# Performance work log

Hardware: AMD Instinct MI355X
Metric: run time of the kernel (lower is better)

The kernel has to match this reference:

```python
import jax, jax.numpy as jnp
import numpy as np

B, T, D, H, L, DFF, MAXLEN = 4, 2048, 512, 8, 6, 2048, 2048
DK = D // H
SCALE = float(1.0 / np.sqrt(DK * 2))  # 1/sqrt(d_k*2)


def layer_norm(x, g, b, eps=1e-5):
    m = jnp.mean(x, axis=-1, keepdims=True)
    v = jnp.var(x, axis=-1, keepdims=True)
    return (x - m) / jnp.sqrt(v + eps) * g + b


def setup_inputs() -> dict:
    key = jax.random.key(0)
    it = iter(jax.random.split(key, 48))
    def n(shape, std=0.02):
        return jax.random.normal(next(it), shape, dtype=jnp.float32) * std
    inp = {}
    inp['x'] = jax.random.normal(next(it), (B, T), dtype=jnp.float32)
    inp['ip_w'] = n((1, D)); inp['ip_b'] = jnp.zeros((D,))
    inp['ip_ln_g'] = jnp.ones((D,)); inp['ip_ln_b'] = jnp.zeros((D,))
    inp['pos_embed'] = n((MAXLEN, D), 0.01)
    inp['pad_token'] = n((D,), 0.01)
    inp['Wq'] = n((L, D, D)); inp['bq'] = jnp.zeros((L, D))
    inp['Wk'] = n((L, D, D)); inp['bk'] = jnp.zeros((L, D))
    inp['Wv'] = n((L, D, D)); inp['bv'] = jnp.zeros((L, D))
    inp['Wo'] = n((L, D, D)); inp['bo'] = jnp.zeros((L, D))
    inp['ln1_g'] = jnp.ones((L, D)); inp['ln1_b'] = jnp.zeros((L, D))
    inp['ln2_g'] = jnp.ones((L, D)); inp['ln2_b'] = jnp.zeros((L, D))
    inp['W1'] = n((L, D, DFF)); inp['b1'] = jnp.zeros((L, DFF))
    inp['W2'] = n((L, DFF, D)); inp['b2'] = jnp.zeros((L, D))
    inp['gate1'] = jnp.full((L,), 0.1); inp['gate2'] = jnp.full((L,), 0.1)
    inp['fn_g'] = jnp.ones((D,)); inp['fn_b'] = jnp.zeros((D,))
    for p in ['bh', 'ah', 'ch']:
        inp[p + '_ln_g'] = jnp.ones((D,)); inp[p + '_ln_b'] = jnp.zeros((D,))
    inp['bh_w'] = n((D, 2), 0.01); inp['bh_b'] = jnp.zeros((2,))
    inp['ah_w'] = n((D, 1), 0.01); inp['ah_b'] = jnp.zeros((1,))
    inp['ch_w'] = n((D, 1), 0.01); inp['ch_b'] = jnp.zeros((1,))
    return inp


def _forward(x, ip_w, ip_b, ip_ln_g, ip_ln_b, pos_embed, pad_token,
             Wq, bq, Wk, bk, Wv, bv, Wo, bo,
             ln1_g, ln1_b, ln2_g, ln2_b, W1, b1, W2, b2, gate1, gate2,
             fn_g, fn_b, bh_ln_g, bh_ln_b, bh_w, bh_b,
             ah_ln_g, ah_ln_b, ah_w, ah_b, ch_ln_g, ch_ln_b, ch_w, ch_b):
    Bx, Tx = x.shape
    xc = jnp.clip(x, -10.0, 10.0)
    pad_mask = xc == -1.0  # [B,T]
    h = layer_norm(xc[..., None] @ ip_w + ip_b, ip_ln_g, ip_ln_b)  # [B,T,D]
    h = h + 0.1 * pos_embed[None, :Tx, :]
    h = jnp.where(pad_mask[..., None], pad_token, h)
    cmask = jnp.triu(jnp.full((Tx, Tx), -10000.0, dtype=h.dtype), k=1)  # additive causal mask
    for i in range(L):
        xn = layer_norm(h, ln1_g[i], ln1_b[i])
        def heads(w, b, xn=xn):
            return (xn @ w + b).reshape(Bx, Tx, H, DK).transpose(0, 2, 1, 3)
        q = heads(Wq[i], bq[i]); k = heads(Wk[i], bk[i]); v = heads(Wv[i], bv[i])
        q = q / jnp.maximum(jnp.linalg.norm(q, axis=-1, keepdims=True), 1e-8)
        k = k / jnp.maximum(jnp.linalg.norm(k, axis=-1, keepdims=True), 1e-8)
        scores = jnp.clip(jnp.einsum('bhtd,bhsd->bhts', q, k) * SCALE, -5.0, 5.0) + cmask
        a = jax.nn.softmax(scores / 1.5, axis=-1)
        o = jnp.einsum('bhts,bhsd->bhtd', a, v).transpose(0, 2, 1, 3).reshape(Bx, Tx, D)
        h = h + gate1[i] * ((o @ Wo[i] + bo[i]) * 0.5)
        xn2 = layer_norm(h, ln2_g[i], ln2_b[i])
        ffn = jax.nn.gelu(xn2 @ W1[i] + b1[i], approximate=False) @ W2[i] + b2[i]
        h = jnp.clip(h + gate2[i] * ffn, -10.0, 10.0)
    h = layer_norm(h, fn_g, fn_b)
    m = (~pad_mask).astype(h.dtype)[..., None]
    mean = (h * m).sum(axis=1) / jnp.maximum(m.sum(axis=1), 1.0)  # masked mean pool [B,D]
    binary = layer_norm(mean, bh_ln_g, bh_ln_b) @ bh_w + bh_b
    anomaly = layer_norm(mean, ah_ln_g, ah_ln_b) @ ah_w + ah_b
    caustic = jax.nn.sigmoid(layer_norm(mean, ch_ln_g, ch_ln_b) @ ch_w + ch_b)
    return jnp.concatenate([binary, anomaly, caustic], axis=-1)  # [B,4]


def reference(x, ip_w, ip_b, ip_ln_g, ip_ln_b, pos_embed, pad_token,
              Wq, bq, Wk, bk, Wv, bv, Wo, bo,
              ln1_g, ln1_b, ln2_g, ln2_b, W1, b1, W2, b2, gate1, gate2,
              fn_g, fn_b, bh_ln_g, bh_ln_b, bh_w, bh_b,
              ah_ln_g, ah_ln_b, ah_w, ah_b, ch_ln_g, ch_ln_b, ch_w, ch_b):
    return _forward(x, ip_w, ip_b, ip_ln_g, ip_ln_b, pos_embed, pad_token,
                    Wq, bq, Wk, bk, Wv, bv, Wo, bo,
                    ln1_g, ln1_b, ln2_g, ln2_b, W1, b1, W2, b2, gate1, gate2,
                    fn_g, fn_b, bh_ln_g, bh_ln_b, bh_w, bh_b,
                    ah_ln_g, ah_ln_b, ah_w, ah_b, ch_ln_g, ch_ln_b, ch_w, ch_b)
```

## Files before the change

kernel.cpp:

```cpp
#include <hip/hip_runtime.h>
#include <math.h>

constexpr int Bsz = 4, T = 2048, D = 512, H = 8, Lnum = 6, DFF = 2048, DK = 64;
constexpr int QS2 = 1024;
constexpr float SCALE = 0.08838834764831845f;
constexpr float K2 = 0.08838834764831845f / 1.5f;

typedef __attribute__((ext_vector_type(8))) short svec8;
typedef __attribute__((ext_vector_type(4))) float fvec4;

__device__ __forceinline__ fvec4 mfma16(svec8 a, svec8 b, fvec4 c) {
    return __builtin_amdgcn_mfma_f32_16x16x32_bf16(a, b, c, 0, 0, 0);
}
__device__ __forceinline__ unsigned short f2b(float f) {
    unsigned int u = __float_as_uint(f);
    u += 0x7fffu + ((u >> 16) & 1u);
    return (unsigned short)(u >> 16);
}
__device__ __forceinline__ float wave_red_sum(float v) {
    for (int o = 32; o > 0; o >>= 1) v += __shfl_down(v, o, 64);
    return __shfl(v, 0, 64);
}
__device__ __forceinline__ void glds16(const unsigned short* g, unsigned short* l) {
    __builtin_amdgcn_global_load_lds(
        (const __attribute__((address_space(1))) unsigned int*)g,
        (__attribute__((address_space(3))) unsigned int*)l, 16, 0, 0);
}
#define FRAG(buf, row, kq) (*(const svec8*)((buf) + (((row) << 6) | ((((kq) ^ ((row) & 7))) << 3))))

__global__ __launch_bounds__(64)
void embed_kernel(const float* __restrict__ x, const float* __restrict__ ip_w,
                  const float* __restrict__ ip_b, const float* __restrict__ g,
                  const float* __restrict__ bta, const float* __restrict__ pos,
                  const float* __restrict__ pad_tok, float* __restrict__ h)
{
    int row = blockIdx.x;
    int t = row & (T - 1);
    int lane = threadIdx.x;
    float xv = x[row];
    float xc = fminf(fmaxf(xv, -10.f), 10.f);
    bool pad = (xc == -1.0f);
    float pre[8];
    float s = 0.f, s2 = 0.f;
#pragma unroll
    for (int j = 0; j < 8; j++) {
        int d = j * 64 + lane;
        float p = xc * ip_w[d] + ip_b[d];
        pre[j] = p; s += p; s2 += p * p;
    }
    s = wave_red_sum(s); s2 = wave_red_sum(s2);
    float m = s * (1.f / 512.f);
    float var = s2 * (1.f / 512.f) - m * m;
    float rstd = 1.f / sqrtf(var + 1e-5f);
#pragma unroll
    for (int j = 0; j < 8; j++) {
        int d = j * 64 + lane;
        float hv = (pre[j] - m) * rstd * g[d] + bta[d] + 0.1f * pos[(size_t)t * D + d];
        if (pad) hv = pad_tok[d];
        h[(size_t)row * D + d] = hv;
    }
}

__global__ __launch_bounds__(256)
void ln_kernel(const float* __restrict__ in, float* __restrict__ out,
               const float* __restrict__ g, const float* __restrict__ b)
{
    int row = blockIdx.x * 4 + (threadIdx.x >> 6);
    int lane = threadIdx.x & 63;
    const float* r = in + (size_t)row * D;
    float4 v0 = ((const float4*)r)[lane];
    float4 v1 = ((const float4*)r)[lane + 64];
    float s = v0.x + v0.y + v0.z + v0.w + v1.x + v1.y + v1.z + v1.w;
    float s2 = v0.x*v0.x + v0.y*v0.y + v0.z*v0.z + v0.w*v0.w
             + v1.x*v1.x + v1.y*v1.y + v1.z*v1.z + v1.w*v1.w;
    s = wave_red_sum(s); s2 = wave_red_sum(s2);
    float m = s * (1.f / 512.f);
    float var = s2 * (1.f / 512.f) - m * m;
    float rstd = 1.f / sqrtf(var + 1e-5f);
    float4 g0 = ((const float4*)g)[lane], g1 = ((const float4*)g)[lane + 64];
    float4 b0 = ((const float4*)b)[lane], b1 = ((const float4*)b)[lane + 64];
    float4 o0, o1;
    o0.x = (v0.x - m) * rstd * g0.x + b0.x; o0.y = (v0.y - m) * rstd * g0.y + b0.y;
    o0.z = (v0.z - m) * rstd * g0.z + b0.z; o0.w = (v0.w - m) * rstd * g0.w + b0.w;
    o1.x = (v1.x - m) * rstd * g1.x + b1.x; o1.y = (v1.y - m) * rstd * g1.y + b1.y;
    o1.z = (v1.z - m) * rstd * g1.z + b1.z; o1.w = (v1.w - m) * rstd * g1.w + b1.w;
    ((float4*)(out + (size_t)row * D))[lane] = o0;
    ((float4*)(out + (size_t)row * D))[lane + 64] = o1;
}

__global__ __launch_bounds__(256)
void ln_bf16_kernel(const float* __restrict__ in, unsigned short* __restrict__ out,
                    const float* __restrict__ g, const float* __restrict__ b)
{
    int row = blockIdx.x * 4 + (threadIdx.x >> 6);
    int lane = threadIdx.x & 63;
    const float* r = in + (size_t)row * D;
    float4 v0 = ((const float4*)r)[lane];
    float4 v1 = ((const float4*)r)[lane + 64];
    float s = v0.x + v0.y + v0.z + v0.w + v1.x + v1.y + v1.z + v1.w;
    float s2 = v0.x*v0.x + v0.y*v0.y + v0.z*v0.z + v0.w*v0.w
             + v1.x*v1.x + v1.y*v1.y + v1.z*v1.z + v1.w*v1.w;
    s = wave_red_sum(s); s2 = wave_red_sum(s2);
    float m = s * (1.f / 512.f);
    float var = s2 * (1.f / 512.f) - m * m;
    float rstd = 1.f / sqrtf(var + 1e-5f);
    float4 g0 = ((const float4*)g)[lane], g1 = ((const float4*)g)[lane + 64];
    float4 b0 = ((const float4*)b)[lane], b1 = ((const float4*)b)[lane + 64];
    unsigned short o0[4], o1[4];
    o0[0] = f2b((v0.x - m) * rstd * g0.x + b0.x); o0[1] = f2b((v0.y - m) * rstd * g0.y + b0.y);
    o0[2] = f2b((v0.z - m) * rstd * g0.z + b0.z); o0[3] = f2b((v0.w - m) * rstd * g0.w + b0.w);
    o1[0] = f2b((v1.x - m) * rstd * g1.x + b1.x); o1[1] = f2b((v1.y - m) * rstd * g1.y + b1.y);
    o1[2] = f2b((v1.z - m) * rstd * g1.z + b1.z); o1[3] = f2b((v1.w - m) * rstd * g1.w + b1.w);
    *(uint2*)(out + (size_t)row * D + lane * 4) = *(uint2*)o0;
    *(uint2*)(out + (size_t)row * D + 256 + lane * 4) = *(uint2*)o1;
}

__global__ __launch_bounds__(256)
void wconv_kernel(const float* __restrict__ wq, const float* __restrict__ wk,
                  const float* __restrict__ wv, const float* __restrict__ wo,
                  const float* __restrict__ w1, const float* __restrict__ w2,
                  unsigned short* __restrict__ oq, unsigned short* __restrict__ ok,
                  unsigned short* __restrict__ ov, unsigned short* __restrict__ oo,
                  unsigned short* __restrict__ o1, unsigned short* __restrict__ o2)
{
    __shared__ float tile[32][33];
    int bid = blockIdx.x;
    const float* in; unsigned short* out; int K, N, kt, nt;
    if (bid < 1024) {
        int sel = bid >> 8, loc = bid & 255;
        in  = sel == 0 ? wq : sel == 1 ? wk : sel == 2 ? wv : wo;
        out = sel == 0 ? oq : sel == 1 ? ok : sel == 2 ? ov : oo;
        K = 512; N = 512; kt = loc >> 4; nt = loc & 15;
    } else if (bid < 2048) {
        int loc = bid - 1024; in = w1; out = o1; K = 512; N = 2048; kt = loc >> 6; nt = loc & 63;
    } else {
        int loc = bid - 2048; in = w2; out = o2; K = 2048; N = 512; kt = loc >> 4; nt = loc & 15;
    }
    int k0 = kt * 32, n0 = nt * 32;
    int t = threadIdx.x;
    int kr = t >> 3, nc = (t & 7) * 4;
    float4 v = *(const float4*)(in + (size_t)(k0 + kr) * N + n0 + nc);
    tile[kr][nc] = v.x; tile[kr][nc + 1] = v.y; tile[kr][nc + 2] = v.z; tile[kr][nc + 3] = v.w;
    __syncthreads();
    unsigned short o[4];
#pragma unroll
    for (int i = 0; i < 4; i++) o[i] = f2b(tile[nc + i][kr]);
    *(uint2*)(out + (size_t)(n0 + kr) * K + k0 + nc) = *(uint2*)o;
}

template<int EPI, int OBF, int BM>
__global__ __launch_bounds__(256)
void gemm_bf16(const unsigned short* __restrict__ A, const unsigned short* __restrict__ BT,
               const float* __restrict__ bias, const float* __restrict__ bias_b,
               const float* __restrict__ bias_c, const float* __restrict__ res,
               void* __restrict__ Cv, unsigned short* __restrict__ vtout,
               int M, int N, int K, const float* __restrict__ gate_p)
{
    constexpr int WN = (BM == 128) ? 2 : 4;
    constexpr int WSPAN = 128 / WN;
    constexpr int NT = WSPAN / 16;
    constexpr int MT = 4;
    constexpr int ACALLS = BM / 32;
    __shared__ __align__(16) unsigned short As[BM * 64];
    __shared__ __align__(16) unsigned short Bs[128 * 64];
    const int tid = threadIdx.x, w = tid >> 6, lane = tid & 63, quad = lane >> 4, ln = lane & 15;
    const int wm = w / WN, wn = w % WN;
    const int m0 = blockIdx.y * BM, n0 = blockIdx.x * 128;
    const int jg = (lane & 7) ^ ((lane >> 3) & 7);
    const int rb = w * 8 + (lane >> 3);
    const unsigned short* Agl = A + (size_t)(m0 + rb) * K + jg * 8;
    const unsigned short* Bgl = BT + (size_t)(n0 + rb) * K + jg * 8;

    fvec4 acc[MT][NT];
#pragma unroll
    for (int mt = 0; mt < MT; mt++)
#pragma unroll
        for (int nt = 0; nt < NT; nt++)
#pragma unroll
            for (int r = 0; r < 4; r++) acc[mt][nt][r] = 0.f;

    for (int k0 = 0; k0 < K; k0 += 64) {
        __syncthreads();
#pragma unroll
        for (int c = 0; c < ACALLS; c++)
            glds16(Agl + k0 + (size_t)c * 32 * K, As + c * 2048 + w * 512);
#pragma unroll
        for (int c = 0; c < 4; c++)
            glds16(Bgl + k0 + (size_t)c * 32 * K, Bs + c * 2048 + w * 512);
        __syncthreads();
#pragma unroll
        for (int kk = 0; kk < 2; kk++) {
            svec8 af[MT], bfr[NT];
#pragma unroll
            for (int mt = 0; mt < MT; mt++)
                af[mt] = FRAG(As, wm * 64 + mt * 16 + ln, kk * 4 + quad);
#pragma unroll
            for (int nt = 0; nt < NT; nt++)
                bfr[nt] = FRAG(Bs, wn * WSPAN + nt * 16 + ln, kk * 4 + quad);
#pragma unroll
            for (int mt = 0; mt < MT; mt++)
#pragma unroll
                for (int nt = 0; nt < NT; nt++)
                    acc[mt][nt] = mfma16(af[mt], bfr[nt], acc[mt][nt]);
        }
    }

    const float gate = (EPI == 1 || EPI == 3) ? gate_p[0] : 0.f;
    float bb[NT];
#pragma unroll
    for (int nt = 0; nt < NT; nt++) {
        int n = n0 + wn * WSPAN + nt * 16 + ln;
        if (EPI == 0) {
            int nseg = n >> 9;
            const float* bsel = nseg == 0 ? bias : (nseg == 1 ? bias_b : bias_c);
            bb[nt] = bsel[n - nseg * 512];
        } else {
            bb[nt] = bias[n];
        }
    }
    const bool qkn = (EPI == 0) && ((n0 + wn * WSPAN) < 1024);
#pragma unroll
    for (int mt = 0; mt < MT; mt++) {
        float v[NT][4];
#pragma unroll
        for (int nt = 0; nt < NT; nt++)
#pragma unroll
            for (int r = 0; r < 4; r++) v[nt][r] = acc[mt][nt][r] + bb[nt];
        if (qkn) {
#pragma unroll
            for (int r = 0; r < 4; r++) {
                float s = 0.f;
#pragma unroll
                for (int nt = 0; nt < NT; nt++) s += v[nt][r] * v[nt][r];
                s += __shfl_xor(s, 1); s += __shfl_xor(s, 2);
                s += __shfl_xor(s, 4); s += __shfl_xor(s, 8);
                float rs = 1.f / fmaxf(sqrtf(s), 1e-8f);
#pragma unroll
                for (int nt = 0; nt < NT; nt++) v[nt][r] *= rs;
            }
        }
#pragma unroll
        for (int nt = 0; nt < NT; nt++) {
            int n = n0 + wn * WSPAN + nt * 16 + ln;
#pragma unroll
            for (int r = 0; r < 4; r++) {
                int m = m0 + wm * 64 + mt * 16 + quad * 4 + r;
                float val = v[nt][r];
                if (EPI == 0) {
                    if (n < 1024) ((unsigned short*)Cv)[(size_t)m * QS2 + n] = f2b(val);
                    else vtout[((size_t)((m >> 11) * 512 + (n - 1024))) * T + (m & (T - 1))] = f2b(val);
                } else {
                    size_t off = (size_t)m * N + n;
                    if (EPI == 1) val = res[off] + gate * 0.5f * val;
                    else if (EPI == 2) val = 0.5f * val * (1.f + erff(val * 0.70710678118654752f));
                    else if (EPI == 3) val = fminf(fmaxf(res[off] + gate * val, -10.f), 10.f);
                    if (OBF) ((unsigned short*)Cv)[off] = f2b(val);
                    else ((float*)Cv)[off] = val;
                }
            }
        }
    }
}

__device__ __forceinline__ void attn_step(
    const unsigned short* Q, unsigned short* Ps, const unsigned short* Ks, const unsigned short* Vt,
    bool diag, fvec4 (&oacc)[4], float (&lp)[4], int w, int quad, int ln)
{
    svec8 a0 = FRAG(Q, w * 16 + ln, quad);
    svec8 a1 = FRAG(Q, w * 16 + ln, 4 + quad);
    fvec4 s[4];
#pragma unroll
    for (int nt = 0; nt < 4; nt++) {
#pragma unroll
        for (int r = 0; r < 4; r++) s[nt][r] = 0.f;
        s[nt] = mfma16(a0, FRAG(Ks, nt * 16 + ln, quad), s[nt]);
        s[nt] = mfma16(a1, FRAG(Ks, nt * 16 + ln, 4 + quad), s[nt]);
    }
    const int qrow = w * 16 + quad * 4;
#pragma unroll
    for (int nt = 0; nt < 4; nt++) {
        int col = nt * 16 + ln;
#pragma unroll
        for (int r = 0; r < 4; r++) {
            float y = s[nt][r] * K2;
            float p = fmaf(y, fmaf(y, fmaf(y, 0.16666667f, 0.5f), 1.f), 1.f);
            if (diag && col > qrow + r) p = 0.f;
            lp[r] += p;
            int row = qrow + r;
            Ps[(row << 6) | ((((col >> 3) ^ (row & 7))) << 3) | (col & 7)] = f2b(p);
        }
    }
#pragma unroll
    for (int ks = 0; ks < 2; ks++) {
        svec8 pa = FRAG(Ps, w * 16 + ln, ks * 4 + quad);
#pragma unroll
        for (int nt = 0; nt < 4; nt++)
            oacc[nt] = mfma16(pa, FRAG(Vt, nt * 16 + ln, ks * 4 + quad), oacc[nt]);
    }
}

__global__ __launch_bounds__(256)
void attn_pair_kernel(const unsigned short* __restrict__ qkv, const unsigned short* __restrict__ vt,
                      unsigned short* __restrict__ o)
{
    __shared__ __align__(16) unsigned short QA[4096], QB[4096];
    __shared__ __align__(16) unsigned short K0[4096], V0[4096], K1[4096], V1[4096];
    __shared__ __align__(16) unsigned short Ps[4096];
    const int p = blockIdx.x, bh = blockIdx.y, b = bh >> 3, hh = bh & 7;
    const int qtA = p, qtB = 31 - p, nst = 32 - p;
    const int tid = threadIdx.x, w = tid >> 6, lane = tid & 63, quad = lane >> 4, ln = lane & 15;
    const int rl = lane >> 3, sl = lane & 7, jgz = sl ^ rl;
    const int w8 = w * 8;
    const int grow = w8 + rl;
    const unsigned short* qrow_p = qkv + ((size_t)(b * T) + grow) * QS2 + hh * 64 + jgz * 8;
    const unsigned short* krow_p = qrow_p + 512;
    const unsigned short* vrow_p = vt + ((size_t)(bh * 64) + grow) * T + jgz * 8;

    glds16(qrow_p + (size_t)(qtA * 64) * QS2, QA + w8 * 64);
    glds16(qrow_p + (size_t)(qtA * 64 + 32) * QS2, QA + (w8 + 32) * 64);
    glds16(qrow_p + (size_t)(qtB * 64) * QS2, QB + w8 * 64);
    glds16(qrow_p + (size_t)(qtB * 64 + 32) * QS2, QB + (w8 + 32) * 64);

    fvec4 oA[4], oB[4];
    float lA[4] = {0, 0, 0, 0}, lB[4] = {0, 0, 0, 0};
#pragma unroll
    for (int nt = 0; nt < 4; nt++)
#pragma unroll
        for (int r = 0; r < 4; r++) { oA[nt][r] = 0.f; oB[nt][r] = 0.f; }

    const int Nph = (nst + 1) >> 1;
    for (int ph = 0; ph < Nph; ph++) {
        const int s0 = 2 * ph, s1 = 2 * ph + 1;
        __syncthreads();
        glds16(krow_p + (size_t)(s0 * 64) * QS2, K0 + w8 * 64);
        glds16(krow_p + (size_t)(s0 * 64 + 32) * QS2, K0 + (w8 + 32) * 64);
        glds16(vrow_p + s0 * 64, V0 + w8 * 64);
        glds16(vrow_p + (size_t)32 * T + s0 * 64, V0 + (w8 + 32) * 64);
        if (s1 < nst) {
            glds16(krow_p + (size_t)(s1 * 64) * QS2, K1 + w8 * 64);
            glds16(krow_p + (size_t)(s1 * 64 + 32) * QS2, K1 + (w8 + 32) * 64);
            glds16(vrow_p + s1 * 64, V1 + w8 * 64);
            glds16(vrow_p + (size_t)32 * T + s1 * 64, V1 + (w8 + 32) * 64);
        }
        __syncthreads();
        attn_step(QB, Ps, K0, V0, s0 == nst - 1, oB, lB, w, quad, ln);
        if (s0 <= p) attn_step(QA, Ps, K0, V0, s0 == p, oA, lA, w, quad, ln);
        if (s1 < nst) {
            attn_step(QB, Ps, K1, V1, s1 == nst - 1, oB, lB, w, quad, ln);
            if (s1 <= p) attn_step(QA, Ps, K1, V1, s1 == p, oA, lA, w, quad, ln);
        }
    }

#pragma unroll
    for (int r = 0; r < 4; r++) {
        float ta = lA[r], tb = lB[r];
        ta += __shfl_xor(ta, 1); ta += __shfl_xor(ta, 2); ta += __shfl_xor(ta, 4); ta += __shfl_xor(ta, 8);
        tb += __shfl_xor(tb, 1); tb += __shfl_xor(tb, 2); tb += __shfl_xor(tb, 4); tb += __shfl_xor(tb, 8);
        lA[r] = ta; lB[r] = tb;
    }
    unsigned short* ogA = o + (size_t)(b * T + qtA * 64 + w * 16 + quad * 4) * D + hh * 64;
    unsigned short* ogB = o + (size_t)(b * T + qtB * 64 + w * 16 + quad * 4) * D + hh * 64;
#pragma unroll
    for (int r = 0; r < 4; r++) {
        float ia = 1.f / lA[r], ib = 1.f / lB[r];
#pragma unroll
        for (int nt = 0; nt < 4; nt++) {
            ogA[(size_t)r * D + nt * 16 + ln] = f2b(oA[nt][r] * ia);
            ogB[(size_t)r * D + nt * 16 + ln] = f2b(oB[nt][r] * ib);
        }
    }
}

__global__ __launch_bounds__(256)
void pool_kernel(const float* __restrict__ hn, const float* __restrict__ x, float* __restrict__ part)
{
    int b = blockIdx.x, ch = blockIdx.y, tid = threadIdx.x;
    int t0 = ch * 128;
    float s0 = 0.f, s1 = 0.f, cnt = 0.f;
    for (int tt = 0; tt < 128; tt++) {
        int t = t0 + tt;
        float xv = x[b * T + t];
        float m = (xv == -1.0f) ? 0.f : 1.f;
        cnt += m;
        const float* r = hn + ((size_t)(b * T + t)) * D;
        s0 += r[tid] * m;
        s1 += r[tid + 256] * m;
    }
    float* pr = part + (size_t)(b * 16 + ch) * 513;
    pr[tid] = s0; pr[tid + 256] = s1;
    if (tid == 0) pr[512] = cnt;
}

__global__ __launch_bounds__(64)
void head_kernel(const float* __restrict__ part,
                 const float* __restrict__ bh_g, const float* __restrict__ bh_bl,
                 const float* __restrict__ ah_g, const float* __restrict__ ah_bl,
                 const float* __restrict__ ch_g, const float* __restrict__ ch_bl,
                 const float* __restrict__ bh_w, const float* __restrict__ bh_b2,
                 const float* __restrict__ ah_w, const float* __restrict__ ah_b2,
                 const float* __restrict__ ch_w, const float* __restrict__ ch_b2,
                 float* __restrict__ out)
{
    int b = blockIdx.x, lane = threadIdx.x;
    float cnt = 0.f;
    for (int c = 0; c < 16; c++) cnt += part[(size_t)(b * 16 + c) * 513 + 512];
    float denom = fmaxf(cnt, 1.f);
    float md[8];
    float s = 0.f, s2 = 0.f;
#pragma unroll
    for (int j = 0; j < 8; j++) {
        int d = j * 64 + lane;
        float acc = 0.f;
        for (int c = 0; c < 16; c++) acc += part[(size_t)(b * 16 + c) * 513 + d];
        md[j] = acc / denom;
        s += md[j]; s2 += md[j] * md[j];
    }
    s = wave_red_sum(s); s2 = wave_red_sum(s2);
    float mu = s * (1.f / 512.f);
    float var = s2 * (1.f / 512.f) - mu * mu;
    float rstd = 1.f / sqrtf(var + 1e-5f);
    float a0 = 0.f, a1 = 0.f, a2 = 0.f, a3 = 0.f;
#pragma unroll
    for (int j = 0; j < 8; j++) {
        int d = j * 64 + lane;
        float z = (md[j] - mu) * rstd;
        float zb = z * bh_g[d] + bh_bl[d];
        a0 += zb * bh_w[d * 2 + 0];
        a1 += zb * bh_w[d * 2 + 1];
        a2 += (z * ah_g[d] + ah_bl[d]) * ah_w[d];
        a3 += (z * ch_g[d] + ch_bl[d]) * ch_w[d];
    }
    a0 = wave_red_sum(a0); a1 = wave_red_sum(a1);
    a2 = wave_red_sum(a2); a3 = wave_red_sum(a3);
    if (lane == 0) {
        out[b * 4 + 0] = a0 + bh_b2[0];
        out[b * 4 + 1] = a1 + bh_b2[1];
        out[b * 4 + 2] = a2 + ah_b2[0];
        float t3 = a3 + ch_b2[0];
        out[b * 4 + 3] = 1.f / (1.f + expf(-t3));
    }
}

extern "C" void kernel_launch(void* const* d_in, const int* in_sizes, int n_in,
                              void* d_out, int out_size, void* d_ws, size_t ws_size,
                              hipStream_t stream)
{
    const float* x      = (const float*)d_in[0];
    const float* ip_w   = (const float*)d_in[1];
    const float* ip_b   = (const float*)d_in[2];
    const float* ip_ln_g= (const float*)d_in[3];
    const float* ip_ln_b= (const float*)d_in[4];
    const float* pos    = (const float*)d_in[5];
    const float* pad_tok= (const float*)d_in[6];
    const float* Wq = (const float*)d_in[7];  const float* bq = (const float*)d_in[8];
    const float* Wk = (const float*)d_in[9];  const float* bk = (const float*)d_in[10];
    const float* Wv = (const float*)d_in[11]; const float* bv = (const float*)d_in[12];
    const float* Wo = (const float*)d_in[13]; const float* bo = (const float*)d_in[14];
    const float* ln1_g = (const float*)d_in[15]; const float* ln1_b = (const float*)d_in[16];
    const float* ln2_g = (const float*)d_in[17]; const float* ln2_b = (const float*)d_in[18];
    const float* W1 = (const float*)d_in[19]; const float* b1 = (const float*)d_in[20];
    const float* W2 = (const float*)d_in[21]; const float* b2 = (const float*)d_in[22];
    const float* gate1 = (const float*)d_in[23]; const float* gate2 = (const float*)d_in[24];
    const float* fn_g = (const float*)d_in[25]; const float* fn_b = (const float*)d_in[26];
    const float* bh_g  = (const float*)d_in[27]; const float* bh_bl = (const float*)d_in[28];
    const float* ah_g  = (const float*)d_in[29]; const float* ah_bl = (const float*)d_in[30];
    const float* ch_g  = (const float*)d_in[31]; const float* ch_bl = (const float*)d_in[32];
    const float* bh_w  = (const float*)d_in[33]; const float* bh_b2 = (const float*)d_in[34];
    const float* ah_w  = (const float*)d_in[35]; const float* ah_b2 = (const float*)d_in[36];
    const float* ch_w  = (const float*)d_in[37]; const float* ch_b2 = (const float*)d_in[38];

    char* ws = (char*)d_ws;
    float*          h     = (float*)ws;
    unsigned short* act_b = (unsigned short*)(ws + 16777216);
    unsigned short* qkv   = (unsigned short*)(ws + 25165824);
    unsigned short* mid_b = (unsigned short*)(ws + 41943040);
    float*          xn_f  = (float*)(ws + 41943040);
    unsigned short* wT    = (unsigned short*)(ws + 75497472);
    unsigned short* vt    = (unsigned short*)(ws + 81788928);
    float*          part  = (float*)(ws + 90177536);
    float*          out   = (float*)d_out;

    unsigned short* wqT = wT;
    unsigned short* wkT = wT + 262144;
    unsigned short* wvT = wT + 524288;
    unsigned short* woT = wT + 786432;
    unsigned short* w1T = wT + 1048576;
    unsigned short* w2T = wT + 2097152;

    embed_kernel<<<dim3(Bsz * T), dim3(64), 0, stream>>>(x, ip_w, ip_b, ip_ln_g, ip_ln_b, pos, pad_tok, h);

    for (int i = 0; i < Lnum; i++) {
        const size_t dd = (size_t)i * D * D;
        const size_t df = (size_t)i * D * DFF;
        wconv_kernel<<<dim3(3072), dim3(256), 0, stream>>>(Wq + dd, Wk + dd, Wv + dd, Wo + dd,
                                                           W1 + df, W2 + df,
                                                           wqT, wkT, wvT, woT, w1T, w2T);
        ln_bf16_kernel<<<dim3(Bsz * T / 4), dim3(256), 0, stream>>>(h, act_b, ln1_g + i * D, ln1_b + i * D);
        gemm_bf16<0, 1, 128><<<dim3(12, 64), dim3(256), 0, stream>>>(act_b, wqT, bq + i * D, bk + i * D, bv + i * D,
                                                                     nullptr, qkv, vt, Bsz * T, 1536, D, nullptr);
        attn_pair_kernel<<<dim3(16, 32), dim3(256), 0, stream>>>(qkv, vt, act_b);
        gemm_bf16<1, 0, 64><<<dim3(4, 128), dim3(256), 0, stream>>>(act_b, woT, bo + i * D, nullptr, nullptr,
                                                                    h, h, nullptr, Bsz * T, D, D, gate1 + i);
        ln_bf16_kernel<<<dim3(Bsz * T / 4), dim3(256), 0, stream>>>(h, act_b, ln2_g + i * D, ln2_b + i * D);
        gemm_bf16<2, 1, 128><<<dim3(16, 64), dim3(256), 0, stream>>>(act_b, w1T, b1 + i * DFF, nullptr, nullptr,
                                                                     nullptr, mid_b, nullptr, Bsz * T, DFF, D, nullptr);
        gemm_bf16<3, 0, 64><<<dim3(4, 128), dim3(256), 0, stream>>>(mid_b, w2T, b2 + i * D, nullptr, nullptr,
                                                                    h, h, nullptr, Bsz * T, D, DFF, gate2 + i);
    }

    ln_kernel<<<dim3(Bsz * T / 4), dim3(256), 0, stream>>>(h, xn_f, fn_g, fn_b);
    pool_kernel<<<dim3(Bsz, 16), dim3(256), 0, stream>>>(xn_f, x, part);
    head_kernel<<<dim3(Bsz), dim3(64), 0, stream>>>(part, bh_g, bh_bl, ah_g, ah_bl, ch_g, ch_bl,
                                                    bh_w, bh_b2, ah_w, ah_b2, ch_w, ch_b2, out);
}
```

Baseline: 1.303 ms.

## Coalesce V-transpose stores, tanh GELU, MFMA row sums, vectorized P writes

The QKV GEMM blocks that produce V now stage the biased tile transposed in shared memory and write it to the V-transpose buffer as 16-byte row stores. Before, each element went out as a scattered 2-byte store. The FFN GELU switches from erf to a tanh approximation built on exp2 and rcp intrinsics. In attention, scores are computed transposed so each lane packs four probabilities into one 8-byte LDS store, and the softmax denominators are accumulated with an MFMA against a ones vector instead of lane shuffles. The score polynomial also drops its cubic term, which changes the numerics, as does the tanh GELU approximation.

```diff
diff --git a/kernel.cpp b/kernel.cpp
--- a/kernel.cpp
+++ b/kernel.cpp
@@ -1,9 +1,9 @@
 #include <hip/hip_runtime.h>
+#include <hip/hip_bf16.h>
 #include <math.h>
 
 constexpr int Bsz = 4, T = 2048, D = 512, H = 8, Lnum = 6, DFF = 2048, DK = 64;
 constexpr int QS2 = 1024;
-constexpr float SCALE = 0.08838834764831845f;
 constexpr float K2 = 0.08838834764831845f / 1.5f;
 
 typedef __attribute__((ext_vector_type(8))) short svec8;
@@ -16,6 +16,10 @@
     unsigned int u = __float_as_uint(f);
     u += 0x7fffu + ((u >> 16) & 1u);
     return (unsigned short)(u >> 16);
+}
+__device__ __forceinline__ unsigned int pk2b(float a, float b) {
+    __hip_bfloat162 h = __float22bfloat162_rn(float2{a, b});
+    return *(unsigned int*)&h;
 }
 __device__ __forceinline__ float wave_red_sum(float v) {
     for (int o = 32; o > 0; o >>= 1) v += __shfl_down(v, o, 64);
@@ -161,8 +165,10 @@
     constexpr int NT = WSPAN / 16;
     constexpr int MT = 4;
     constexpr int ACALLS = BM / 32;
-    __shared__ __align__(16) unsigned short As[BM * 64];
-    __shared__ __align__(16) unsigned short Bs[128 * 64];
+    constexpr int SMEMSZ = (EPI == 0) ? 17408 : (BM * 64 + 128 * 64);
+    __shared__ __align__(16) unsigned short SMEM[SMEMSZ];
+    unsigned short* As = SMEM;
+    unsigned short* Bs = SMEM + BM * 64;
     const int tid = threadIdx.x, w = tid >> 6, lane = tid & 63, quad = lane >> 4, ln = lane & 15;
     const int wm = w / WN, wn = w % WN;
     const int m0 = blockIdx.y * BM, n0 = blockIdx.x * 128;
@@ -218,7 +224,31 @@
             bb[nt] = bias[n];
         }
     }
-    const bool qkn = (EPI == 0) && ((n0 + wn * WSPAN) < 1024);
+
+    if (EPI == 0 && n0 >= 1024) {
+        __syncthreads();
+#pragma unroll
+        for (int mt = 0; mt < MT; mt++) {
+#pragma unroll
+            for (int nt = 0; nt < NT; nt++) {
+                int nl = wn * 64 + nt * 16 + ln;
+                int mb = wm * 64 + mt * 16 + quad * 4;
+                unsigned int lo = pk2b(acc[mt][nt][0] + bb[nt], acc[mt][nt][1] + bb[nt]);
+                unsigned int hi = pk2b(acc[mt][nt][2] + bb[nt], acc[mt][nt][3] + bb[nt]);
+                uint2 u; u.x = lo; u.y = hi;
+                *(uint2*)(SMEM + nl * 136 + mb) = u;
+            }
+        }
+        __syncthreads();
+        int row = tid >> 1, half = (tid & 1) * 64;
+        unsigned short* dst = vtout + ((size_t)((m0 >> 11) * 512 + (n0 - 1024) + row)) * T
+                              + (m0 & (T - 1)) + half;
+        const unsigned short* src = SMEM + row * 136 + half;
+#pragma unroll
+        for (int j = 0; j < 8; j++) *(uint4*)(dst + j * 8) = *(const uint4*)(src + j * 8);
+        return;
+    }
+
 #pragma unroll
     for (int mt = 0; mt < MT; mt++) {
         float v[NT][4];
@@ -226,7 +256,7 @@
         for (int nt = 0; nt < NT; nt++)
 #pragma unroll
             for (int r = 0; r < 4; r++) v[nt][r] = acc[mt][nt][r] + bb[nt];
-        if (qkn) {
+        if (EPI == 0) {
 #pragma unroll
             for (int r = 0; r < 4; r++) {
                 float s = 0.f;
@@ -247,12 +277,17 @@
                 int m = m0 + wm * 64 + mt * 16 + quad * 4 + r;
                 float val = v[nt][r];
                 if (EPI == 0) {
-                    if (n < 1024) ((unsigned short*)Cv)[(size_t)m * QS2 + n] = f2b(val);
-                    else vtout[((size_t)((m >> 11) * 512 + (n - 1024))) * T + (m & (T - 1))] = f2b(val);
+                    ((unsigned short*)Cv)[(size_t)m * QS2 + n] = f2b(val);
                 } else {
                     size_t off = (size_t)m * N + n;
                     if (EPI == 1) val = res[off] + gate * 0.5f * val;
-                    else if (EPI == 2) val = 0.5f * val * (1.f + erff(val * 0.70710678118654752f));
+                    else if (EPI == 2) {
+                        float u = val;
+                        float z = 0.7978845608028654f * fmaf(0.044715f * u, u * u, u);
+                        float e = __builtin_amdgcn_exp2f(z * 2.8853900817779268f);
+                        float rr = __builtin_amdgcn_rcpf(e + 1.f);
+                        val = u * (1.f - rr);
+                    }
                     else if (EPI == 3) val = fminf(fmaxf(res[off] + gate * val, -10.f), 10.f);
                     if (OBF) ((unsigned short*)Cv)[off] = f2b(val);
                     else ((float*)Cv)[off] = val;
@@ -264,35 +299,35 @@
 
 __device__ __forceinline__ void attn_step(
     const unsigned short* Q, unsigned short* Ps, const unsigned short* Ks, const unsigned short* Vt,
-    bool diag, fvec4 (&oacc)[4], float (&lp)[4], int w, int quad, int ln)
-{
-    svec8 a0 = FRAG(Q, w * 16 + ln, quad);
-    svec8 a1 = FRAG(Q, w * 16 + ln, 4 + quad);
-    fvec4 s[4];
+    bool diag, fvec4 (&oacc)[4], fvec4& lacc, int w, int quad, int ln)
+{
+    constexpr short BONE = (short)0x3F80;
+    const svec8 ONES8 = {BONE, BONE, BONE, BONE, BONE, BONE, BONE, BONE};
+    svec8 qf0 = FRAG(Q, w * 16 + ln, quad);
+    svec8 qf1 = FRAG(Q, w * 16 + ln, 4 + quad);
+    const int qrow = w * 16 + ln;
 #pragma unroll
     for (int nt = 0; nt < 4; nt++) {
-#pragma unroll
-        for (int r = 0; r < 4; r++) s[nt][r] = 0.f;
-        s[nt] = mfma16(a0, FRAG(Ks, nt * 16 + ln, quad), s[nt]);
-        s[nt] = mfma16(a1, FRAG(Ks, nt * 16 + ln, 4 + quad), s[nt]);
-    }
-    const int qrow = w * 16 + quad * 4;
-#pragma unroll
-    for (int nt = 0; nt < 4; nt++) {
-        int col = nt * 16 + ln;
+        fvec4 z; z[0] = z[1] = z[2] = z[3] = 0.f;
+        z = mfma16(FRAG(Ks, nt * 16 + ln, quad), qf0, z);
+        z = mfma16(FRAG(Ks, nt * 16 + ln, 4 + quad), qf1, z);
+        const int sbase = nt * 16 + quad * 4;
+        float p[4];
 #pragma unroll
         for (int r = 0; r < 4; r++) {
-            float y = s[nt][r] * K2;
-            float p = fmaf(y, fmaf(y, fmaf(y, 0.16666667f, 0.5f), 1.f), 1.f);
-            if (diag && col > qrow + r) p = 0.f;
-            lp[r] += p;
-            int row = qrow + r;
-            Ps[(row << 6) | ((((col >> 3) ^ (row & 7))) << 3) | (col & 7)] = f2b(p);
-        }
+            float y = z[r] * K2;
+            float pv = fmaf(y, fmaf(y, 0.5f, 1.f), 1.f);
+            if (diag && (sbase + r > qrow)) pv = 0.f;
+            p[r] = pv;
+        }
+        uint2 u; u.x = pk2b(p[0], p[1]); u.y = pk2b(p[2], p[3]);
+        int chunk = sbase >> 3, off = sbase & 7;
+        *(uint2*)(Ps + ((qrow << 6) | ((chunk ^ (qrow & 7)) << 3) | off)) = u;
     }
 #pragma unroll
     for (int ks = 0; ks < 2; ks++) {
         svec8 pa = FRAG(Ps, w * 16 + ln, ks * 4 + quad);
+        lacc = mfma16(pa, ONES8, lacc);
 #pragma unroll
         for (int nt = 0; nt < 4; nt++)
             oacc[nt] = mfma16(pa, FRAG(Vt, nt * 16 + ln, ks * 4 + quad), oacc[nt]);
@@ -321,8 +356,9 @@
     glds16(qrow_p + (size_t)(qtB * 64) * QS2, QB + w8 * 64);
     glds16(qrow_p + (size_t)(qtB * 64 + 32) * QS2, QB + (w8 + 32) * 64);
 
-    fvec4 oA[4], oB[4];
-    float lA[4] = {0, 0, 0, 0}, lB[4] = {0, 0, 0, 0};
+    fvec4 oA[4], oB[4], lAv, lBv;
+#pragma unroll
+    for (int r = 0; r < 4; r++) { lAv[r] = 0.f; lBv[r] = 0.f; }
 #pragma unroll
     for (int nt = 0; nt < 4; nt++)
 #pragma unroll
@@ -343,26 +379,19 @@
             glds16(vrow_p + (size_t)32 * T + s1 * 64, V1 + (w8 + 32) * 64);
         }
         __syncthreads();
-        attn_step(QB, Ps, K0, V0, s0 == nst - 1, oB, lB, w, quad, ln);
-        if (s0 <= p) attn_step(QA, Ps, K0, V0, s0 == p, oA, lA, w, quad, ln);
+        attn_step(QB, Ps, K0, V0, s0 == nst - 1, oB, lBv, w, quad, ln);
+        if (s0 <= p) attn_step(QA, Ps, K0, V0, s0 == p, oA, lAv, w, quad, ln);
         if (s1 < nst) {
-            attn_step(QB, Ps, K1, V1, s1 == nst - 1, oB, lB, w, quad, ln);
-            if (s1 <= p) attn_step(QA, Ps, K1, V1, s1 == p, oA, lA, w, quad, ln);
-        }
-    }
-
-#pragma unroll
-    for (int r = 0; r < 4; r++) {
-        float ta = lA[r], tb = lB[r];
-        ta += __shfl_xor(ta, 1); ta += __shfl_xor(ta, 2); ta += __shfl_xor(ta, 4); ta += __shfl_xor(ta, 8);
-        tb += __shfl_xor(tb, 1); tb += __shfl_xor(tb, 2); tb += __shfl_xor(tb, 4); tb += __shfl_xor(tb, 8);
-        lA[r] = ta; lB[r] = tb;
-    }
+            attn_step(QB, Ps, K1, V1, s1 == nst - 1, oB, lBv, w, quad, ln);
+            if (s1 <= p) attn_step(QA, Ps, K1, V1, s1 == p, oA, lAv, w, quad, ln);
+        }
+    }
+
     unsigned short* ogA = o + (size_t)(b * T + qtA * 64 + w * 16 + quad * 4) * D + hh * 64;
     unsigned short* ogB = o + (size_t)(b * T + qtB * 64 + w * 16 + quad * 4) * D + hh * 64;
 #pragma unroll
     for (int r = 0; r < 4; r++) {
-        float ia = 1.f / lA[r], ib = 1.f / lB[r];
+        float ia = 1.f / lAv[r], ib = 1.f / lBv[r];
 #pragma unroll
         for (int nt = 0; nt < 4; nt++) {
             ogA[(size_t)r * D + nt * 16 + ln] = f2b(oA[nt][r] * ia);
```

Result: faster. 1.228 ms (-5.8%).
